# Kernel tuning notes

Hardware: AMD Instinct MI355X
Metric: run time of the kernel (lower is better)

The kernel has to match this reference:

```python
import jax, jax.numpy as jnp
import numpy as np

NUM_CLASSES = 10
CLS_W, L1_W, GIOU_W = 2.0, 5.0, 2.0


def box_cxcywh_to_xyxy(b):
    cx, cy, w, h = b[..., 0], b[..., 1], b[..., 2], b[..., 3]
    return jnp.stack([cx - w / 2, cy - h / 2, cx + w / 2, cy + h / 2], axis=-1)


def giou_matrix(b1, b2):
    # b1: (B,N,4), b2: (B,M,4) xyxy -> (B,N,M)
    a1 = jnp.clip(b1[..., 2] - b1[..., 0], 0) * jnp.clip(b1[..., 3] - b1[..., 1], 0)
    a2 = jnp.clip(b2[..., 2] - b2[..., 0], 0) * jnp.clip(b2[..., 3] - b2[..., 1], 0)
    lt = jnp.maximum(b1[..., :, None, :2], b2[..., None, :, :2])
    rb = jnp.minimum(b1[..., :, None, 2:], b2[..., None, :, 2:])
    wh = jnp.clip(rb - lt, 0)
    inter = wh[..., 0] * wh[..., 1]
    union = a1[..., :, None] + a2[..., None, :] - inter
    iou = inter / jnp.clip(union, 1e-6)
    lte = jnp.minimum(b1[..., :, None, :2], b2[..., None, :, :2])
    rbe = jnp.maximum(b1[..., :, None, 2:], b2[..., None, :, 2:])
    whe = jnp.clip(rbe - lte, 0)
    enc = whe[..., 0] * whe[..., 1]
    return iou - (enc - union) / jnp.clip(enc, 1e-6)


def giou_elem(b1, b2):
    # b1, b2: (N,4) xyxy, paired -> (N,)
    a1 = jnp.clip(b1[:, 2] - b1[:, 0], 0) * jnp.clip(b1[:, 3] - b1[:, 1], 0)
    a2 = jnp.clip(b2[:, 2] - b2[:, 0], 0) * jnp.clip(b2[:, 3] - b2[:, 1], 0)
    lt = jnp.maximum(b1[:, :2], b2[:, :2])
    rb = jnp.minimum(b1[:, 2:], b2[:, 2:])
    wh = jnp.clip(rb - lt, 0)
    inter = wh[:, 0] * wh[:, 1]
    union = a1 + a2 - inter
    iou = inter / jnp.clip(union, 1e-6)
    lte = jnp.minimum(b1[:, :2], b2[:, :2])
    rbe = jnp.maximum(b1[:, 2:], b2[:, 2:])
    whe = jnp.clip(rbe - lte, 0)
    enc = whe[:, 0] * whe[:, 1]
    return iou - (enc - union) / jnp.clip(enc, 1e-6)


def hungarian(cost):
    # Jonker-Volgenant style shortest-augmenting-path assignment (== scipy.linear_sum_assignment)
    cost = np.asarray(cost, dtype=np.float64)
    transposed = cost.shape[0] > cost.shape[1]
    C = cost.T if transposed else cost
    n, m = C.shape  # n <= m
    u = np.zeros(n + 1)
    v = np.zeros(m + 1)
    p = np.zeros(m + 1, dtype=np.int64)
    colr = np.arange(m + 1)
    for i in range(1, n + 1):
        p[0] = i
        j0 = 0
        minv = np.full(m + 1, np.inf)
        way = np.zeros(m + 1, dtype=np.int64)
        used = np.zeros(m + 1, dtype=bool)
        while True:
            used[j0] = True
            i0 = p[j0]
            unused = colr[1:][~used[1:]]
            cur = C[i0 - 1, unused - 1] - u[i0] - v[unused]
            better = cur < minv[unused]
            bidx = unused[better]
            minv[bidx] = cur[better]
            way[bidx] = j0
            j1 = unused[np.argmin(minv[unused])]
            delta = minv[j1]
            u[p[used]] += delta
            v[used] -= delta
            minv[~used] -= delta
            j0 = j1
            if p[j0] == 0:
                break
        while j0 != 0:
            jn = way[j0]
            p[j0] = p[jn]
            j0 = jn
    rows = p[1:] - 1
    cols = np.arange(m)
    sel = rows >= 0
    r, c = rows[sel], cols[sel]
    if transposed:
        r, c = c, r
    order = np.argsort(r)
    return r[order], c[order]


def compute_matches(pred_logits, pred_boxes, gt_classes, gt_boxes):
    # Batched cost matrices on device, per-sample Hungarian on host (mirrors torch.no_grad matcher).
    B, Q, _ = pred_logits.shape
    G = gt_classes.shape[1]
    prob = jax.nn.softmax(pred_logits, axis=-1)
    cls_idx = jnp.clip(gt_classes, 0, NUM_CLASSES - 1)
    idx = jnp.broadcast_to(cls_idx[:, None, :], (B, Q, G))
    cls_cost = -jnp.take_along_axis(prob, idx, axis=2)                 # (B,Q,G)
    l1_cost = jnp.abs(pred_boxes[:, :, None, :] - gt_boxes[:, None, :, :]).sum(-1)
    g = giou_matrix(box_cxcywh_to_xyxy(pred_boxes), box_cxcywh_to_xyxy(gt_boxes))
    cost = CLS_W * cls_cost + L1_W * l1_cost - GIOU_W * g
    cost_np = np.asarray(jax.device_get(cost))
    valid_np = np.asarray(jax.device_get(gt_classes)) >= 0
    bs, ps, gs = [], [], []
    for bi in range(B):
        vidx = np.nonzero(valid_np[bi])[0]
        if vidx.size == 0:
            continue
        r, c = hungarian(cost_np[bi][:, vidx])
        bs.append(np.full(r.size, bi, dtype=np.int64))
        ps.append(r.astype(np.int64))
        gs.append(vidx[c].astype(np.int64))
    if bs:
        return np.concatenate(bs), np.concatenate(ps), np.concatenate(gs)
    z = np.zeros(0, np.int64)
    return z, z, z


def detection_loss(pred_logits, pred_boxes, gt_boxes, target_cls, b_f, p_f, g_f, n_matched):
    C1 = pred_logits.shape[-1]
    logp = jax.nn.log_softmax(pred_logits, axis=-1).reshape(-1, C1)
    t = target_cls.reshape(-1)
    w = jnp.ones(C1, dtype=pred_logits.dtype).at[-1].set(0.1)
    nll = -jnp.take_along_axis(logp, t[:, None], axis=1)[:, 0]
    wt = w[t]
    cls_loss = (wt * nll).sum() / wt.sum()
    mp = pred_boxes[b_f, p_f]
    mg = gt_boxes[b_f, g_f]
    l1 = jnp.abs(mp - mg).sum()
    gd = giou_elem(box_cxcywh_to_xyxy(mp), box_cxcywh_to_xyxy(mg))
    gl = (1.0 - gd).sum()
    return CLS_W * cls_loss + L1_W * l1 / n_matched + GIOU_W * gl / n_matched


def setup_inputs() -> dict:
    key = jax.random.key(0)
    k1, k2, k3, k4, k5 = jax.random.split(key, 5)
    B, Q, G, C = 64, 900, 100, NUM_CLASSES
    pred_logits = jax.random.normal(k1, (B, Q, C + 1), dtype=jnp.float32)
    pred_boxes = jax.random.uniform(k2, (B, Q, 4), dtype=jnp.float32, minval=0.05, maxval=0.6)
    gt_boxes = jax.random.uniform(k3, (B, G, 4), dtype=jnp.float32, minval=0.05, maxval=0.6)
    cls = jax.random.randint(k4, (B, G), 0, C)
    nvalid = jax.random.randint(k5, (B,), 1, G + 1)
    mask = jnp.arange(G)[None, :] < nvalid[:, None]
    gt_classes = jnp.where(mask, cls, -1).astype(jnp.int32)
    return {"pred_logits": pred_logits, "pred_boxes": pred_boxes,
            "gt_classes": gt_classes, "gt_boxes": gt_boxes}


def reference(pred_logits, pred_boxes, gt_classes, gt_boxes):
    B, Q = pred_logits.shape[:2]
    b_f, p_f, g_f = compute_matches(pred_logits, pred_boxes, gt_classes, gt_boxes)
    gt_np = np.asarray(jax.device_get(gt_classes))
    tc = np.full((B, Q), NUM_CLASSES, dtype=np.int32)
    tc[b_f, p_f] = gt_np[b_f, g_f]
    n_matched = max(int(b_f.size), 1)
    return detection_loss(pred_logits, pred_boxes, gt_boxes, jnp.asarray(tc), b_f, p_f, g_f, n_matched)
```

## Files before the change

### kernel.cpp

```cpp
#include <hip/hip_runtime.h>
#include <hip/hip_bf16.h>
#include <math.h>

#define BB 64
#define QQ 900
#define GG 100
#define NCLS 10
#define CP1 11

#define STRIDE 960
#define KPL 15
#define NT 512
#define NW 8
#define QMASK 255
#define ROUND_CAP 20000

#define CLS_W 2.0f
#define L1_W 5.0f
#define GIOU_W 2.0f

struct Accum {
  double wnll, wt, l1, gl;
  int nm, counter;
  int pad[6];
};

__global__ __launch_bounds__(256) void cost_kernel(
    const float* __restrict__ logits, const float* __restrict__ pboxes,
    const int* __restrict__ gcls, const float* __restrict__ gboxes,
    float* __restrict__ cost, Accum* acc) {
  const int b = blockIdx.y;
  const int q = blockIdx.x * 256 + threadIdx.x;

  if (blockIdx.x == 0 && blockIdx.y == 0 && threadIdx.x == 0) {
    acc->wnll = 0.0; acc->wt = 0.0; acc->l1 = 0.0; acc->gl = 0.0;
    acc->nm = 0; acc->counter = 0;
  }

  __shared__ float s_gb[GG * 4];
  __shared__ int   s_gc[GG];
  __shared__ float s_prob[256 * 13];

  for (int i = threadIdx.x; i < GG * 4; i += 256) s_gb[i] = gboxes[b * GG * 4 + i];
  for (int i = threadIdx.x; i < GG; i += 256)     s_gc[i] = gcls[b * GG + i];

  float pcx = 0.f, pcy = 0.f, pw = 0.f, ph = 0.f;
  if (q < QQ) {
    const float* lg = logits + ((size_t)b * QQ + q) * CP1;
    float l[CP1];
    float mx = -1e30f;
    for (int c = 0; c < CP1; ++c) { l[c] = lg[c]; mx = fmaxf(mx, l[c]); }
    float se = 0.f;
    for (int c = 0; c < CP1; ++c) { l[c] = expf(l[c] - mx); se += l[c]; }
    float inv = 1.0f / se;
    for (int c = 0; c < CP1; ++c) s_prob[threadIdx.x * 13 + c] = l[c] * inv;
    const float* pb = pboxes + ((size_t)b * QQ + q) * 4;
    pcx = pb[0]; pcy = pb[1]; pw = pb[2]; ph = pb[3];
  }
  __syncthreads();
  if (q >= STRIDE) return;

  float* crow = cost + ((size_t)b * GG) * STRIDE + q;
  if (q >= QQ) {
    for (int g = 0; g < GG; ++g) crow[(size_t)g * STRIDE] = 1e30f;
    return;
  }

  const float px1 = pcx - 0.5f * pw, py1 = pcy - 0.5f * ph;
  const float px2 = pcx + 0.5f * pw, py2 = pcy + 0.5f * ph;
  const float pa = fmaxf(px2 - px1, 0.f) * fmaxf(py2 - py1, 0.f);

  for (int g = 0; g < GG; ++g) {
    int cls = s_gc[g];
    cls = cls < 0 ? 0 : (cls > NCLS - 1 ? NCLS - 1 : cls);
    const float cc = -s_prob[threadIdx.x * 13 + cls];
    const float gcx = s_gb[g * 4 + 0], gcy = s_gb[g * 4 + 1];
    const float gw  = s_gb[g * 4 + 2], gh  = s_gb[g * 4 + 3];
    const float l1 = fabsf(pcx - gcx) + fabsf(pcy - gcy) + fabsf(pw - gw) + fabsf(ph - gh);
    const float gx1 = gcx - 0.5f * gw, gy1 = gcy - 0.5f * gh;
    const float gx2 = gcx + 0.5f * gw, gy2 = gcy + 0.5f * gh;
    const float ga = fmaxf(gx2 - gx1, 0.f) * fmaxf(gy2 - gy1, 0.f);
    const float ltx = fmaxf(px1, gx1), lty = fmaxf(py1, gy1);
    const float rbx = fminf(px2, gx2), rby = fminf(py2, gy2);
    const float iw = fmaxf(rbx - ltx, 0.f), ih = fmaxf(rby - lty, 0.f);
    const float inter = iw * ih;
    const float uni = pa + ga - inter;
    const float iou = inter / fmaxf(uni, 1e-6f);
    const float ex1 = fminf(px1, gx1), ey1 = fminf(py1, gy1);
    const float ex2 = fmaxf(px2, gx2), ey2 = fmaxf(py2, gy2);
    const float ew = fmaxf(ex2 - ex1, 0.f), eh = fmaxf(ey2 - ey1, 0.f);
    const float enc = ew * eh;
    const float giou = iou - (enc - uni) / fmaxf(enc, 1e-6f);
    crow[(size_t)g * STRIDE] = CLS_W * cc + L1_W * l1 - GIOU_W * giou;
  }
}

__global__ __launch_bounds__(NT) void jv_kernel(
    const float* __restrict__ logits, const float* __restrict__ pboxes,
    const int* __restrict__ gcls, const float* __restrict__ gboxes,
    const float* __restrict__ cost, Accum* acc, float* out) {
  const int b = blockIdx.x;
  const int tid = threadIdx.x;
  const int lane = tid & 63;
  const int w = tid >> 6;

  __shared__ float vl[STRIDE + 2];
  __shared__ int   p[QQ + 1];
  __shared__ int   way[STRIDE + 2];
  __shared__ float m1l[GG + 1], m2l[GG + 1];
  __shared__ int   aminl[GG + 1];
  __shared__ int   s_gc[GG];
  __shared__ int   queue[QMASK + 1];
  __shared__ int   sh_n, sh_qtail;
  __shared__ double r0[NW], r1[NW], r2[NW], r3[NW];
  __shared__ int r4[NW];

  if (tid == 0) { sh_n = 0; sh_qtail = 0; }
  for (int j = tid; j <= QQ; j += NT) p[j] = 0;
  for (int j = tid; j < STRIDE + 2; j += NT) { vl[j] = 0.f; way[j] = 0x7FFFFFFF; }
  if (tid < GG) s_gc[tid] = gcls[b * GG + tid];
  __syncthreads();
  if (tid < GG && s_gc[tid] >= 0) atomicAdd(&sh_n, 1);
  __syncthreads();
  const int n = sh_n;
  const float* Cb = cost + (size_t)b * GG * STRIDE;

  for (int r = w; r < n; r += NW) {
    const float* Cr = Cb + (size_t)r * STRIDE + lane;
    float rca[KPL];
#pragma unroll
    for (int k = 0; k < KPL; ++k) rca[k] = Cr[k << 6];
    float m1 = 3e38f, m2 = 3e38f, n1 = 3e38f, n2 = 3e38f;
    int j1 = 0x7FFFFFFF, i1 = 0x7FFFFFFF;
#pragma unroll
    for (int k = 0; k < 8; ++k) {
      const float c = rca[k];
      if (c < m1) { m2 = m1; m1 = c; j1 = 1 + lane + (k << 6); }
      else if (c < m2) m2 = c;
    }
#pragma unroll
    for (int k = 8; k < KPL; ++k) {
      const float c = rca[k];
      if (c < n1) { n2 = n1; n1 = c; i1 = 1 + lane + (k << 6); }
      else if (c < n2) n2 = c;
    }
    if (n1 < m1) { m2 = fminf(m1, n2); m1 = n1; j1 = i1; }
    else m2 = fminf(m2, n1);
    for (int m = 1; m < 64; m <<= 1) {
      const float o1 = __shfl_xor(m1, m);
      const float o2 = __shfl_xor(m2, m);
      const int oj = __shfl_xor(j1, m);
      if (o1 < m1) { m2 = fminf(m1, o2); m1 = o1; j1 = oj; }
      else m2 = fminf(m2, o1);
    }
    if (lane == 0) { m1l[r] = m1; m2l[r] = m2; aminl[r] = j1; }
  }
  __syncthreads();

  if (tid < n) atomicMin(&way[aminl[tid]], tid);
  __syncthreads();
  if (tid < n) {
    const int j1 = aminl[tid];
    if (way[j1] == tid) {
      p[j1] = tid + 1;
      vl[j1] = m1l[tid] - m2l[tid];
    } else {
      const int t0 = atomicAdd(&sh_qtail, 1);
      queue[t0 & QMASK] = tid + 1;
    }
  }
  __syncthreads();

  if (w == 0) {
    float v[KPL], rc[KPL];
#pragma unroll
    for (int k = 0; k < KPL; ++k) v[k] = vl[1 + lane + (k << 6)];
    int head = 0, tail = sh_qtail, rounds = 0;
    int cur = -1;
    if (head < tail) {
      cur = queue[head & QMASK];
      const float* Cr = Cb + (size_t)(cur - 1) * STRIDE + lane;
#pragma unroll
      for (int k = 0; k < KPL; ++k) rc[k] = Cr[k << 6];
    }
    while (head < tail && rounds < ROUND_CAP) {
      const int i = cur;
      head++;
      float m1 = 3e38f, m2 = 3e38f, n1 = 3e38f, n2 = 3e38f;
      int j1 = 0x7FFFFFFF, i1 = 0x7FFFFFFF;
#pragma unroll
      for (int k = 0; k < 8; ++k) {
        const float c = rc[k] - v[k];
        if (c < m1) { m2 = m1; m1 = c; j1 = 1 + lane + (k << 6); }
        else if (c < m2) m2 = c;
      }
#pragma unroll
      for (int k = 8; k < KPL; ++k) {
        const float c = rc[k] - v[k];
        if (c < n1) { n2 = n1; n1 = c; i1 = 1 + lane + (k << 6); }
        else if (c < n2) n2 = c;
      }
      if (n1 < m1) { m2 = fminf(m1, n2); m1 = n1; j1 = i1; }
      else m2 = fminf(m2, n1);
      for (int m = 1; m < 64; m <<= 1) {
        const float o1 = __shfl_xor(m1, m);
        const float o2 = __shfl_xor(m2, m);
        const int oj = __shfl_xor(j1, m);
        if (o1 < m1) { m2 = fminf(m1, o2); m1 = o1; j1 = oj; }
        else m2 = fminf(m2, o1);
      }
      float d = m2 - m1;
      if (d < 0.f) d = 0.f;
      const int c0 = j1 - 1;
      if ((c0 & 63) == lane) {
        const int kk = c0 >> 6;
        const float ov = v[kk];
        float nv = ov - d;
        if (!(nv < ov)) nv = nextafterf(ov, -3e38f);
        v[kk] = nv;
      }
      const int k0 = p[j1];
      p[j1] = i;
      if (k0 > 0) {
        if (lane == 0) queue[tail & QMASK] = k0;
        tail++;
      }
      cur = -1;
      if (head < tail) {
        cur = queue[head & QMASK];
        const float* Cr = Cb + (size_t)(cur - 1) * STRIDE + lane;
#pragma unroll
        for (int k = 0; k < KPL; ++k) rc[k] = Cr[k << 6];
      }
      rounds++;
    }
  }
  __syncthreads();

  double wnll = 0.0, wt = 0.0, l1d = 0.0, gld = 0.0;
  int nm = 0;
  for (int q = tid; q < QQ; q += NT) {
    const int idx = b * QQ + q;
    const float* lg = logits + (size_t)idx * CP1;
    float l[CP1];
    float mx = -1e30f;
    for (int c = 0; c < CP1; ++c) { l[c] = lg[c]; mx = fmaxf(mx, l[c]); }
    float se = 0.f;
    for (int c = 0; c < CP1; ++c) se += expf(l[c] - mx);
    const float lse = logf(se);
    const int g = p[q + 1] - 1;
    const int t = (g >= 0) ? s_gc[g] : NCLS;
    float lt = l[0];
    for (int c = 1; c < CP1; ++c) lt = (c == t) ? l[c] : lt;
    const float logp = (lt - mx) - lse;
    const float wgt = (t == NCLS) ? 0.1f : 1.0f;
    wnll += (double)(wgt * (-logp));
    wt += (double)wgt;
    if (g >= 0) {
      nm += 1;
      const float* pb = pboxes + (size_t)idx * 4;
      const float* gb = gboxes + ((size_t)b * GG + g) * 4;
      const float pcx = pb[0], pcy = pb[1], pw = pb[2], ph = pb[3];
      const float gcx = gb[0], gcy = gb[1], gw = gb[2], gh = gb[3];
      const float l1 = fabsf(pcx - gcx) + fabsf(pcy - gcy) + fabsf(pw - gw) + fabsf(ph - gh);
      const float px1 = pcx - 0.5f * pw, py1 = pcy - 0.5f * ph;
      const float px2 = pcx + 0.5f * pw, py2 = pcy + 0.5f * ph;
      const float gx1 = gcx - 0.5f * gw, gy1 = gcy - 0.5f * gh;
      const float gx2 = gcx + 0.5f * gw, gy2 = gcy + 0.5f * gh;
      const float pa = fmaxf(px2 - px1, 0.f) * fmaxf(py2 - py1, 0.f);
      const float ga = fmaxf(gx2 - gx1, 0.f) * fmaxf(gy2 - gy1, 0.f);
      const float ltx = fmaxf(px1, gx1), lty = fmaxf(py1, gy1);
      const float rbx = fminf(px2, gx2), rby = fminf(py2, gy2);
      const float iw = fmaxf(rbx - ltx, 0.f), ih = fmaxf(rby - lty, 0.f);
      const float inter = iw * ih;
      const float uni = pa + ga - inter;
      const float iou = inter / fmaxf(uni, 1e-6f);
      const float ex1 = fminf(px1, gx1), ey1 = fminf(py1, gy1);
      const float ex2 = fmaxf(px2, gx2), ey2 = fmaxf(py2, gy2);
      const float ew = fmaxf(ex2 - ex1, 0.f), eh = fmaxf(ey2 - ey1, 0.f);
      const float enc = ew * eh;
      const float giou = iou - (enc - uni) / fmaxf(enc, 1e-6f);
      l1d += (double)l1;
      gld += (double)(1.0f - giou);
    }
  }

  for (int off = 32; off; off >>= 1) {
    wnll += __shfl_down(wnll, off);
    wt   += __shfl_down(wt, off);
    l1d  += __shfl_down(l1d, off);
    gld  += __shfl_down(gld, off);
    nm   += __shfl_down(nm, off);
  }
  if (lane == 0) { r0[w] = wnll; r1[w] = wt; r2[w] = l1d; r3[w] = gld; r4[w] = nm; }
  __syncthreads();
  if (tid == 0) {
    for (int x = 1; x < NW; ++x) { wnll += r0[x]; wt += r1[x]; l1d += r2[x]; gld += r3[x]; nm += r4[x]; }
    atomicAdd(&acc->wnll, wnll);
    atomicAdd(&acc->wt, wt);
    atomicAdd(&acc->l1, l1d);
    atomicAdd(&acc->gl, gld);
    atomicAdd(&acc->nm, nm);
    __threadfence();
    const int ticket = atomicAdd(&acc->counter, 1);
    if (ticket == BB - 1) {
      const double fw = atomicAdd(&acc->wnll, 0.0);
      const double fwt = atomicAdd(&acc->wt, 0.0);
      const double fl1 = atomicAdd(&acc->l1, 0.0);
      const double fgl = atomicAdd(&acc->gl, 0.0);
      int fnm = atomicAdd(&acc->nm, 0);
      if (fnm < 1) fnm = 1;
      const double loss = (double)CLS_W * (fw / fwt) +
                          ((double)L1_W * fl1 + (double)GIOU_W * fgl) / (double)fnm;
      out[0] = (float)loss;
    }
  }
}

extern "C" void kernel_launch(void* const* d_in, const int* in_sizes, int n_in,
                              void* d_out, int out_size, void* d_ws, size_t ws_size,
                              hipStream_t stream) {
  const float* logits = (const float*)d_in[0];
  const float* pboxes = (const float*)d_in[1];
  const int*   gcls   = (const int*)d_in[2];
  const float* gboxes = (const float*)d_in[3];

  char* ws = (char*)d_ws;
  Accum* acc = (Accum*)ws;
  float* cost = (float*)(ws + 128);

  cost_kernel<<<dim3((STRIDE + 255) / 256, BB), 256, 0, stream>>>(logits, pboxes, gcls, gboxes, cost, acc);
  jv_kernel<<<BB, NT, 0, stream>>>(logits, pboxes, gcls, gboxes, cost, acc, (float*)d_out);
}
```

Baseline: 123.7 us.

## Prefetch queued cost rows three deep and resolve initial column conflicts by regret

The serial auction loop in wave 0 now keeps three register buffers of upcoming queued rows, so global loads for future rows are issued ahead of the current step and their latency is hidden. Initial column conflicts are now resolved by a packed 64-bit atomicMax keyed on each row's regret (second-best minus best) instead of the lowest row index. The intent is to cut memory stalls in the sequential loop and reduce how many rows get re-queued. In exchange the loop has three times the register footprint, and a prefetched row goes stale if the queue order changes.

```diff
diff --git a/kernel.cpp b/kernel.cpp
--- a/kernel.cpp
+++ b/kernel.cpp
@@ -106,7 +106,7 @@
 
   __shared__ float vl[STRIDE + 2];
   __shared__ int   p[QQ + 1];
-  __shared__ int   way[STRIDE + 2];
+  __shared__ unsigned long long way64[STRIDE + 2];
   __shared__ float m1l[GG + 1], m2l[GG + 1];
   __shared__ int   aminl[GG + 1];
   __shared__ int   s_gc[GG];
@@ -117,7 +117,7 @@
 
   if (tid == 0) { sh_n = 0; sh_qtail = 0; }
   for (int j = tid; j <= QQ; j += NT) p[j] = 0;
-  for (int j = tid; j < STRIDE + 2; j += NT) { vl[j] = 0.f; way[j] = 0x7FFFFFFF; }
+  for (int j = tid; j < STRIDE + 2; j += NT) { vl[j] = 0.f; way64[j] = 0ull; }
   if (tid < GG) s_gc[tid] = gcls[b * GG + tid];
   __syncthreads();
   if (tid < GG && s_gc[tid] >= 0) atomicAdd(&sh_n, 1);
@@ -157,11 +157,16 @@
   }
   __syncthreads();
 
-  if (tid < n) atomicMin(&way[aminl[tid]], tid);
+  if (tid < n) {
+    const float regret = m2l[tid] - m1l[tid];
+    const unsigned long long key =
+        ((unsigned long long)__float_as_uint(regret) << 20) | (unsigned long long)(tid + 1);
+    atomicMax(&way64[aminl[tid]], key);
+  }
   __syncthreads();
   if (tid < n) {
     const int j1 = aminl[tid];
-    if (way[j1] == tid) {
+    if ((int)(way64[j1] & 0xFFFFFu) == tid + 1) {
       p[j1] = tid + 1;
       vl[j1] = m1l[tid] - m2l[tid];
     } else {
@@ -172,20 +177,20 @@
   __syncthreads();
 
   if (w == 0) {
-    float v[KPL], rc[KPL];
+    float v[KPL];
 #pragma unroll
     for (int k = 0; k < KPL; ++k) v[k] = vl[1 + lane + (k << 6)];
     int head = 0, tail = sh_qtail, rounds = 0;
-    int cur = -1;
-    if (head < tail) {
-      cur = queue[head & QMASK];
-      const float* Cr = Cb + (size_t)(cur - 1) * STRIDE + lane;
-#pragma unroll
-      for (int k = 0; k < KPL; ++k) rc[k] = Cr[k << 6];
-    }
-    while (head < tail && rounds < ROUND_CAP) {
-      const int i = cur;
-      head++;
+
+    float bufA[KPL], bufB[KPL], bufC[KPL];
+    int ia = -1, ib = -1, ic = -1;
+
+    auto loadrow = [&](float* buf, int rid) {
+      const float* Cr = Cb + (size_t)(rid - 1) * STRIDE + lane;
+#pragma unroll
+      for (int k = 0; k < KPL; ++k) buf[k] = Cr[k << 6];
+    };
+    auto do_step = [&](float* rc, int i) {
       float m1 = 3e38f, m2 = 3e38f, n1 = 3e38f, n2 = 3e38f;
       int j1 = 0x7FFFFFFF, i1 = 0x7FFFFFFF;
 #pragma unroll
@@ -221,17 +226,34 @@
       }
       const int k0 = p[j1];
       p[j1] = i;
+      head++;
       if (k0 > 0) {
         if (lane == 0) queue[tail & QMASK] = k0;
         tail++;
       }
-      cur = -1;
-      if (head < tail) {
-        cur = queue[head & QMASK];
-        const float* Cr = Cb + (size_t)(cur - 1) * STRIDE + lane;
-#pragma unroll
-        for (int k = 0; k < KPL; ++k) rc[k] = Cr[k << 6];
-      }
+    };
+
+    if (head < tail)     { ia = queue[head & QMASK];       loadrow(bufA, ia); }
+    if (head + 1 < tail) { ib = queue[(head + 1) & QMASK]; loadrow(bufB, ib); }
+    if (head + 2 < tail) { ic = queue[(head + 2) & QMASK]; loadrow(bufC, ic); }
+
+    while (head < tail && rounds < ROUND_CAP) {
+      if (ia < 0) { ia = queue[head & QMASK]; loadrow(bufA, ia); }
+      do_step(bufA, ia);
+      ia = -1;
+      if (head + 2 < tail) { ia = queue[(head + 2) & QMASK]; loadrow(bufA, ia); }
+      rounds++;
+      if (!(head < tail && rounds < ROUND_CAP)) break;
+      if (ib < 0) { ib = queue[head & QMASK]; loadrow(bufB, ib); }
+      do_step(bufB, ib);
+      ib = -1;
+      if (head + 2 < tail) { ib = queue[(head + 2) & QMASK]; loadrow(bufB, ib); }
+      rounds++;
+      if (!(head < tail && rounds < ROUND_CAP)) break;
+      if (ic < 0) { ic = queue[head & QMASK]; loadrow(bufC, ic); }
+      do_step(bufC, ic);
+      ic = -1;
+      if (head + 2 < tail) { ic = queue[(head + 2) & QMASK]; loadrow(bufC, ic); }
       rounds++;
     }
   }
```

New measurement: 118.3 us. -4.3%, faster.

## Process displaced rows depth-first and prefetch next queued row in auction loop

Applied to the files above, without the earlier changes.

The serial auction/JV loop now follows a displaced row immediately (depth-first) instead of appending it to the FIFO queue, and issues its cost-row load right after the argmin reduction. The next queued row is prefetched into a second register buffer so its global load overlaps with the current row's work. The initial conflict resolution now gives each contested column to the row with the largest regret via a 64-bit atomicMax, and reductions break ties by lowest index. This targets global-load latency on the single-wavefront critical path and aims for fewer reassignment rounds, at the cost of extra registers and a changed processing order that may alter which assignment is found when costs tie.

```diff
diff --git a/kernel.cpp b/kernel.cpp
--- a/kernel.cpp
+++ b/kernel.cpp
@@ -12,7 +12,6 @@
 #define KPL 15
 #define NT 512
 #define NW 8
-#define QMASK 255
 #define ROUND_CAP 20000
 
 #define CLS_W 2.0f
@@ -106,18 +105,18 @@
 
   __shared__ float vl[STRIDE + 2];
   __shared__ int   p[QQ + 1];
-  __shared__ int   way[STRIDE + 2];
+  __shared__ unsigned long long way64[STRIDE + 2];
   __shared__ float m1l[GG + 1], m2l[GG + 1];
   __shared__ int   aminl[GG + 1];
   __shared__ int   s_gc[GG];
-  __shared__ int   queue[QMASK + 1];
+  __shared__ int   queue[GG + 4];
   __shared__ int   sh_n, sh_qtail;
   __shared__ double r0[NW], r1[NW], r2[NW], r3[NW];
   __shared__ int r4[NW];
 
   if (tid == 0) { sh_n = 0; sh_qtail = 0; }
   for (int j = tid; j <= QQ; j += NT) p[j] = 0;
-  for (int j = tid; j < STRIDE + 2; j += NT) { vl[j] = 0.f; way[j] = 0x7FFFFFFF; }
+  for (int j = tid; j < STRIDE + 2; j += NT) { vl[j] = 0.f; way64[j] = 0ull; }
   if (tid < GG) s_gc[tid] = gcls[b * GG + tid];
   __syncthreads();
   if (tid < GG && s_gc[tid] >= 0) atomicAdd(&sh_n, 1);
@@ -150,42 +149,55 @@
       const float o1 = __shfl_xor(m1, m);
       const float o2 = __shfl_xor(m2, m);
       const int oj = __shfl_xor(j1, m);
-      if (o1 < m1) { m2 = fminf(m1, o2); m1 = o1; j1 = oj; }
+      if (o1 < m1 || (o1 == m1 && oj < j1)) { m2 = fminf(m1, o2); m1 = o1; j1 = oj; }
       else m2 = fminf(m2, o1);
     }
     if (lane == 0) { m1l[r] = m1; m2l[r] = m2; aminl[r] = j1; }
   }
   __syncthreads();
 
-  if (tid < n) atomicMin(&way[aminl[tid]], tid);
+  if (tid < n) {
+    const float regret = m2l[tid] - m1l[tid];
+    const unsigned long long key =
+        ((unsigned long long)__float_as_uint(regret) << 20) | (unsigned long long)(tid + 1);
+    atomicMax(&way64[aminl[tid]], key);
+  }
   __syncthreads();
   if (tid < n) {
     const int j1 = aminl[tid];
-    if (way[j1] == tid) {
+    if ((int)(way64[j1] & 0xFFFFFu) == tid + 1) {
       p[j1] = tid + 1;
       vl[j1] = m1l[tid] - m2l[tid];
     } else {
-      const int t0 = atomicAdd(&sh_qtail, 1);
-      queue[t0 & QMASK] = tid + 1;
+      queue[atomicAdd(&sh_qtail, 1)] = tid + 1;
     }
   }
   __syncthreads();
 
   if (w == 0) {
-    float v[KPL], rc[KPL];
+    float v[KPL];
 #pragma unroll
     for (int k = 0; k < KPL; ++k) v[k] = vl[1 + lane + (k << 6)];
-    int head = 0, tail = sh_qtail, rounds = 0;
-    int cur = -1;
+    int head = 0;
+    const int tail = sh_qtail;
+    float rc[KPL], qb[KPL];
+    int cur = -1, qnext = -1;
     if (head < tail) {
-      cur = queue[head & QMASK];
+      cur = queue[head]; head++;
       const float* Cr = Cb + (size_t)(cur - 1) * STRIDE + lane;
 #pragma unroll
       for (int k = 0; k < KPL; ++k) rc[k] = Cr[k << 6];
     }
-    while (head < tail && rounds < ROUND_CAP) {
+    if (head < tail) {
+      qnext = queue[head]; head++;
+      const float* Cr = Cb + (size_t)(qnext - 1) * STRIDE + lane;
+#pragma unroll
+      for (int k = 0; k < KPL; ++k) qb[k] = Cr[k << 6];
+    }
+    int steps = 0;
+    while (cur > 0 && steps < ROUND_CAP) {
+      steps++;
       const int i = cur;
-      head++;
       float m1 = 3e38f, m2 = 3e38f, n1 = 3e38f, n2 = 3e38f;
       int j1 = 0x7FFFFFFF, i1 = 0x7FFFFFFF;
 #pragma unroll
@@ -202,12 +214,20 @@
       }
       if (n1 < m1) { m2 = fminf(m1, n2); m1 = n1; j1 = i1; }
       else m2 = fminf(m2, n1);
+      int pl = p[j1];
       for (int m = 1; m < 64; m <<= 1) {
         const float o1 = __shfl_xor(m1, m);
         const float o2 = __shfl_xor(m2, m);
-        const int oj = __shfl_xor(j1, m);
-        if (o1 < m1) { m2 = fminf(m1, o2); m1 = o1; j1 = oj; }
+        const int   oj = __shfl_xor(j1, m);
+        const int   op = __shfl_xor(pl, m);
+        if (o1 < m1 || (o1 == m1 && oj < j1)) { m2 = fminf(m1, o2); m1 = o1; j1 = oj; pl = op; }
         else m2 = fminf(m2, o1);
+      }
+      const int k0 = pl;
+      if (k0 > 0) {
+        const float* Cr = Cb + (size_t)(k0 - 1) * STRIDE + lane;
+#pragma unroll
+        for (int k = 0; k < KPL; ++k) rc[k] = Cr[k << 6];
       }
       float d = m2 - m1;
       if (d < 0.f) d = 0.f;
@@ -219,20 +239,23 @@
         if (!(nv < ov)) nv = nextafterf(ov, -3e38f);
         v[kk] = nv;
       }
-      const int k0 = p[j1];
       p[j1] = i;
       if (k0 > 0) {
-        if (lane == 0) queue[tail & QMASK] = k0;
-        tail++;
-      }
-      cur = -1;
-      if (head < tail) {
-        cur = queue[head & QMASK];
-        const float* Cr = Cb + (size_t)(cur - 1) * STRIDE + lane;
-#pragma unroll
-        for (int k = 0; k < KPL; ++k) rc[k] = Cr[k << 6];
-      }
-      rounds++;
+        cur = k0;
+      } else {
+        cur = qnext;
+        if (cur > 0) {
+#pragma unroll
+          for (int k = 0; k < KPL; ++k) rc[k] = qb[k];
+          qnext = -1;
+          if (head < tail) {
+            qnext = queue[head]; head++;
+            const float* Cr = Cb + (size_t)(qnext - 1) * STRIDE + lane;
+#pragma unroll
+            for (int k = 0; k < KPL; ++k) qb[k] = Cr[k << 6];
+          }
+        }
+      }
     }
   }
   __syncthreads();
```

New measurement: 125.9 us. About the same (+1.8%).
